# Kernel optimization log

Measured on AMD Instinct MI355X. Metric: run time of the kernel, lower is better.

Reference implementation:

```python
import jax, jax.numpy as jnp
import numpy as np

E = 512       # embed_dim
H = 8         # num_heads
DH = E // H   # head dim
F = 2048      # dim_feedforward
KS = 33       # NATTEN kernel_size (dilation=1)
NCLS = 1
B = 2
L = 4096      # local tokens (total seq = L + NCLS)
EPS = 1e-5


def layernorm(x, g, b):
    mu = jnp.mean(x, axis=-1, keepdims=True)
    var = jnp.mean(jnp.square(x - mu), axis=-1, keepdims=True)
    return (x - mu) * jax.lax.rsqrt(var + EPS) * g + b


def natten_1d(x, qkv_w, qkv_b, proj_w, proj_b):
    # Neighborhood attention 1D, dilation=1, non-causal, no rel-pos bias.
    b, l, e = x.shape
    qkv = x @ qkv_w.T + qkv_b                       # [b, l, 3E]
    q, k, v = jnp.split(qkv, 3, axis=-1)
    q = q.reshape(b, l, H, DH) * (DH ** -0.5)
    k = k.reshape(b, l, H, DH)
    v = v.reshape(b, l, H, DH)
    # NATTEN window: centered, shifted at edges to keep exactly KS in-bounds neighbors
    starts = jnp.clip(jnp.arange(l) - KS // 2, 0, l - KS)   # [l]
    idx = starts[:, None] + jnp.arange(KS)                  # [l, KS]
    kn = k[:, idx]                                          # [b, l, KS, H, DH]
    vn = v[:, idx]                                          # [b, l, KS, H, DH]
    attn = jnp.einsum('blhd,blkhd->bhlk', q, kn)
    attn = jax.nn.softmax(attn, axis=-1)
    out = jnp.einsum('bhlk,blkhd->blhd', attn, vn).reshape(b, l, e)
    return out @ proj_w.T + proj_b


def global_mha(q_in, kv_in, in_w, in_b, out_w, out_b):
    # torch nn.MultiheadAttention, batch_first, no masks
    bq, lq, e = q_in.shape
    lk = kv_in.shape[1]
    wq, wk, wv = jnp.split(in_w, 3, axis=0)
    bqp, bkp, bvp = jnp.split(in_b, 3, axis=0)
    q = (q_in @ wq.T + bqp).reshape(bq, lq, H, DH) * (DH ** -0.5)
    k = (kv_in @ wk.T + bkp).reshape(bq, lk, H, DH)
    v = (kv_in @ wv.T + bvp).reshape(bq, lk, H, DH)
    attn = jax.nn.softmax(jnp.einsum('bqhd,bkhd->bhqk', q, k), axis=-1)
    out = jnp.einsum('bhqk,bkhd->bqhd', attn, v).reshape(bq, lq, e)
    return out @ out_w.T + out_b


def setup_inputs() -> dict:
    key = jax.random.key(0)
    ks = jax.random.split(key, 16)
    s = 0.02
    return {
        'x': jax.random.normal(ks[0], (B, L + NCLS, E), jnp.float32),
        'ln1_g': jnp.ones((E,), jnp.float32),
        'ln1_b': jnp.zeros((E,), jnp.float32),
        'qkv_w': jax.random.normal(ks[1], (3 * E, E), jnp.float32) * s,
        'qkv_b': jnp.zeros((3 * E,), jnp.float32),
        'na_proj_w': jax.random.normal(ks[2], (E, E), jnp.float32) * s,
        'na_proj_b': jnp.zeros((E,), jnp.float32),
        'in_proj_w': jax.random.normal(ks[3], (3 * E, E), jnp.float32) * s,
        'in_proj_b': jnp.zeros((3 * E,), jnp.float32),
        'out_w': jax.random.normal(ks[4], (E, E), jnp.float32) * s,
        'out_b': jnp.zeros((E,), jnp.float32),
        'ln2_g': jnp.ones((E,), jnp.float32),
        'ln2_b': jnp.zeros((E,), jnp.float32),
        'fc1_w': jax.random.normal(ks[5], (F, E), jnp.float32) * s,
        'fc1_b': jnp.zeros((F,), jnp.float32),
        'fc2_w': jax.random.normal(ks[6], (E, F), jnp.float32) * s,
        'fc2_b': jnp.zeros((E,), jnp.float32),
    }


def reference(x, ln1_g, ln1_b, qkv_w, qkv_b, na_proj_w, na_proj_b,
              in_proj_w, in_proj_b, out_w, out_b, ln2_g, ln2_b,
              fc1_w, fc1_b, fc2_w, fc2_b):
    res = x
    xn = layernorm(x, ln1_g, ln1_b)
    x_local = natten_1d(xn[:, :-NCLS, :], qkv_w, qkv_b, na_proj_w, na_proj_b)
    tmp_key = jnp.concatenate([x_local, xn[:, -NCLS:, :]], axis=1)
    x_cls = global_mha(xn[:, -NCLS:, :], tmp_key, in_proj_w, in_proj_b, out_w, out_b)
    x = res + jnp.concatenate([x_local, x_cls], axis=1)
    res = x
    xn = layernorm(x, ln2_g, ln2_b)
    h = jax.nn.silu(xn @ fc1_w.T + fc1_b)
    return res + (h @ fc2_w.T + fc2_b)
```

## Files before the change

### kernel.cpp

```cpp
#include <hip/hip_runtime.h>
#include <hip/hip_bf16.h>
#include <cstdint>
#include <cstddef>

#define E    512
#define H    8
#define DHD  64
#define FDIM 2048
#define KS   33
#define BB   2
#define LL   4096
#define LP1  4097
#define NTOK 8194
#define NLOC 8192

typedef unsigned short ushort_t;
typedef __bf16 bf16x8_t __attribute__((ext_vector_type(8)));
typedef float  f32x4_t  __attribute__((ext_vector_type(4)));

__device__ __forceinline__ float b2f(unsigned short h) {
  union { unsigned int u; float f; } un; un.u = ((unsigned int)h) << 16; return un.f;
}
__device__ __forceinline__ unsigned short f2b(float f) {
  union { float f; unsigned int u; } un; un.f = f;
  unsigned int u = un.u;
  return (unsigned short)((u + 0x7FFFu + ((u >> 16) & 1u)) >> 16);
}

__device__ __forceinline__ void gload16(const ushort_t* g, ushort_t* l) {
  __builtin_amdgcn_global_load_lds(
      (const __attribute__((address_space(1))) void*)g,
      (__attribute__((address_space(3))) void*)l,
      16, 0, 0);
}

template<int N> __device__ __forceinline__ void waitcnt_vm() {
  if constexpr (N == 8)      asm volatile("s_waitcnt vmcnt(8)" ::: "memory");
  else if constexpr (N == 6) asm volatile("s_waitcnt vmcnt(6)" ::: "memory");
  else                       asm volatile("s_waitcnt vmcnt(0)" ::: "memory");
}

__device__ __forceinline__ int xcd_remap(int hw, int n) {
  int xcd = hw & 7, j = hw >> 3;
  int q = n >> 3, r = n & 7;
  return (xcd < r ? xcd * (q + 1) : r * (q + 1) + (xcd - r) * q) + j;
}

template<int BMT, int BNT, int NTH, int WC, int ACT, int OUTF, int ADDRES,
         int INRM, int OUTRM, int PARTIAL>
__global__ __launch_bounds__(NTH) void gemm_bt(
    const ushort_t* __restrict__ A, const ushort_t* __restrict__ W,
    const float* __restrict__ bias, float* __restrict__ outF,
    ushort_t* __restrict__ outB, const ushort_t* __restrict__ res,
    int M, int N, int K, int klen, int ny, int nz, size_t pstr)
{
  constexpr int WR  = NTH / 64 / WC;
  constexpr int MF  = BMT / (WR * 16);
  constexpr int NF  = BNT / (WC * 16);
  constexpr int AR  = (BMT * 64) / (8 * NTH);
  constexpr int BR  = (BNT * 64) / (8 * NTH);
  constexpr int RPR = NTH / 8;
  constexpr int NLD = AR + BR;
  __shared__ ushort_t Alds[2][BMT * 64];
  __shared__ ushort_t Blds[2][BNT * 64];
  const int t    = threadIdx.x;
  const int lane = t & 63;
  const int w    = t >> 6;
  const int wr   = w / WC, wc = w % WC;

  const int Lid = xcd_remap(blockIdx.x, gridDim.x);
  const int bx  = Lid / (ny * nz);
  const int rem = Lid % (ny * nz);
  const int z   = rem / ny;
  const int by  = rem % ny;
  const int bmBase = bx * BMT;
  const int bnBase = by * BNT;
  const int kbeg = z * klen;

  f32x4_t zero = {0.f, 0.f, 0.f, 0.f};
  f32x4_t acc[MF][NF];
  #pragma unroll
  for (int m = 0; m < MF; ++m)
    #pragma unroll
    for (int n = 0; n < NF; ++n) acc[m][n] = zero;

  const int srow = t >> 3;
  const int jsw8 = ((t & 7) ^ (srow & 7)) * 8;
  int arow[AR];
  #pragma unroll
  for (int r = 0; r < AR; ++r) {
    int rr = bmBase + r * RPR + srow;
    if (INRM) rr += rr >> 12;
    else if (rr >= M) rr = M - 1;
    arow[r] = rr;
  }
  int brow[BR];
  #pragma unroll
  for (int r = 0; r < BR; ++r) brow[r] = bnBase + r * RPR + srow;

  const int frow = lane & 15;
  const int g    = lane >> 4;

  auto STAGE = [&](int s, int k0) {
    #pragma unroll
    for (int r = 0; r < AR; ++r)
      gload16(A + (size_t)arow[r] * K + k0 + jsw8, &Alds[s][(size_t)(r * NTH + t) * 8]);
    #pragma unroll
    for (int r = 0; r < BR; ++r)
      gload16(W + (size_t)brow[r] * K + k0 + jsw8, &Blds[s][(size_t)(r * NTH + t) * 8]);
  };

  const int nt = klen >> 6;
  STAGE(0, kbeg);
  if (nt > 1) STAGE(1, kbeg + 64);

  for (int it = 0; it < nt; ++it) {
    const int cur = it & 1;
    if (it < nt - 1) waitcnt_vm<NLD>();
    else             waitcnt_vm<0>();
    __builtin_amdgcn_s_barrier();
    #pragma unroll
    for (int kk2 = 0; kk2 < 2; ++kk2) {
      bf16x8_t af[MF], bfv[NF];
      const int kosw = ((kk2 * 4 + g) ^ (frow & 7)) << 4;
      #pragma unroll
      for (int m = 0; m < MF; ++m) {
        int row = wr * (MF * 16) + m * 16 + frow;
        af[m] = *reinterpret_cast<const bf16x8_t*>((char*)Alds[cur] + row * 128 + kosw);
      }
      #pragma unroll
      for (int n = 0; n < NF; ++n) {
        int row = wc * (NF * 16) + n * 16 + frow;
        bfv[n] = *reinterpret_cast<const bf16x8_t*>((char*)Blds[cur] + row * 128 + kosw);
      }
      #pragma unroll
      for (int m = 0; m < MF; ++m)
        #pragma unroll
        for (int n = 0; n < NF; ++n)
          acc[m][n] = __builtin_amdgcn_mfma_f32_16x16x32_bf16(af[m], bfv[n], acc[m][n], 0, 0, 0);
    }
    __builtin_amdgcn_s_barrier();
    if (it + 2 < nt) STAGE(cur, kbeg + (it + 2) * 64);
  }

  const int rbase = g * 4;
  const int cbase = frow;
  #pragma unroll
  for (int m = 0; m < MF; ++m) {
    #pragma unroll
    for (int r = 0; r < 4; ++r) {
      int gr = bmBase + wr * (MF * 16) + m * 16 + rbase + r;
      if (gr < M) {
        int orow = OUTRM ? gr + (gr >> 12) : gr;
        #pragma unroll
        for (int n = 0; n < NF; ++n) {
          int gc = bnBase + wc * (NF * 16) + n * 16 + cbase;
          float v = acc[m][n][r];
          if (PARTIAL) {
            outB[(size_t)z * pstr + (size_t)orow * N + gc] = f2b(v);
          } else {
            v += bias[gc];
            if (ACT == 1) v = v / (1.f + __expf(-v));
            if (ADDRES) v += b2f(res[(size_t)gr * N + gc]);
            if (OUTF) outF[(size_t)orow * N + gc] = v;
            else      outB[(size_t)orow * N + gc] = f2b(v);
          }
        }
      }
    }
  }
}

template<int NP>
__global__ __launch_bounds__(256) void fc2_reduce(
    float* __restrict__ out, const ushort_t* __restrict__ parts, size_t pstr,
    const float* __restrict__ bias, const ushort_t* __restrict__ xab)
{
  size_t i4 = (size_t)blockIdx.x * 256 + threadIdx.x;
  ushort4 xv = reinterpret_cast<const ushort4*>(xab)[i4];
  float4 bcol = reinterpret_cast<const float4*>(bias)[i4 & 127];
  float4 o;
  o.x = b2f(xv.x) + bcol.x; o.y = b2f(xv.y) + bcol.y;
  o.z = b2f(xv.z) + bcol.z; o.w = b2f(xv.w) + bcol.w;
  #pragma unroll
  for (int zp = 0; zp < NP; ++zp) {
    ushort4 pv = *reinterpret_cast<const ushort4*>(parts + (size_t)zp * pstr + i4 * 4);
    o.x += b2f(pv.x); o.y += b2f(pv.y); o.z += b2f(pv.z); o.w += b2f(pv.w);
  }
  reinterpret_cast<float4*>(out)[i4] = o;
}

__global__ __launch_bounds__(256) void ln_fused1(
    const float* __restrict__ x, const float* __restrict__ g,
    const float* __restrict__ be, ushort_t* __restrict__ xn,
    ushort_t* __restrict__ tmpk)
{
  __shared__ float sh[4];
  const int row = blockIdx.x;
  const int t = threadIdx.x;
  const float* xr = x + (size_t)row * E;
  float v0 = xr[t], v1 = xr[t + 256];
  float sum = v0 + v1;
  #pragma unroll
  for (int o = 32; o; o >>= 1) sum += __shfl_xor(sum, o);
  if ((t & 63) == 0) sh[t >> 6] = sum;
  __syncthreads();
  float mean = (sh[0] + sh[1] + sh[2] + sh[3]) * (1.f / E);
  __syncthreads();
  float d0 = v0 - mean, d1 = v1 - mean;
  float vs = d0 * d0 + d1 * d1;
  #pragma unroll
  for (int o = 32; o; o >>= 1) vs += __shfl_xor(vs, o);
  if ((t & 63) == 0) sh[t >> 6] = vs;
  __syncthreads();
  float var = (sh[0] + sh[1] + sh[2] + sh[3]) * (1.f / E);
  float rstd = rsqrtf(var + 1e-5f);
  unsigned short o0 = f2b(d0 * rstd * g[t] + be[t]);
  unsigned short o1 = f2b(d1 * rstd * g[t + 256] + be[t + 256]);
  xn[(size_t)row * E + t] = o0;
  xn[(size_t)row * E + t + 256] = o1;
  if ((row % LP1) == LL) {
    tmpk[(size_t)row * E + t] = o0;
    tmpk[(size_t)row * E + t + 256] = o1;
  }
}

__global__ __launch_bounds__(256) void resid_ln2(
    const float* __restrict__ x, const ushort_t* __restrict__ tmpk,
    const float* __restrict__ xcls, const float* __restrict__ g,
    const float* __restrict__ be, ushort_t* __restrict__ xab,
    ushort_t* __restrict__ xn2)
{
  __shared__ float sh[4];
  const int row = blockIdx.x;
  const int b = row / LP1, l = row % LP1;
  const int t = threadIdx.x;
  float a0, a1;
  if (l < LL) { a0 = b2f(tmpk[(size_t)row * E + t]); a1 = b2f(tmpk[(size_t)row * E + t + 256]); }
  else        { a0 = xcls[b * E + t];                a1 = xcls[b * E + t + 256]; }
  float v0 = x[(size_t)row * E + t] + a0;
  float v1 = x[(size_t)row * E + t + 256] + a1;
  xab[(size_t)row * E + t] = f2b(v0);
  xab[(size_t)row * E + t + 256] = f2b(v1);
  float sum = v0 + v1;
  #pragma unroll
  for (int o = 32; o; o >>= 1) sum += __shfl_xor(sum, o);
  if ((t & 63) == 0) sh[t >> 6] = sum;
  __syncthreads();
  float mean = (sh[0] + sh[1] + sh[2] + sh[3]) * (1.f / E);
  __syncthreads();
  float d0 = v0 - mean, d1 = v1 - mean;
  float vs = d0 * d0 + d1 * d1;
  #pragma unroll
  for (int o = 32; o; o >>= 1) vs += __shfl_xor(vs, o);
  if ((t & 63) == 0) sh[t >> 6] = vs;
  __syncthreads();
  float var = (sh[0] + sh[1] + sh[2] + sh[3]) * (1.f / E);
  float rstd = rsqrtf(var + 1e-5f);
  xn2[(size_t)row * E + t]       = f2b(d0 * rstd * g[t] + be[t]);
  xn2[(size_t)row * E + t + 256] = f2b(d1 * rstd * g[t + 256] + be[t + 256]);
}

__global__ __launch_bounds__(256) void natten_mfma(
    const ushort_t* __restrict__ qkv, ushort_t* __restrict__ out)
{
  __shared__ ushort_t KP[4][64 * 64];
  __shared__ ushort_t VT[4][64 * 72];
  const int w    = threadIdx.x >> 6;
  const int lane = threadIdx.x & 63;
  const int task = blockIdx.x * 4 + w;
  const int h  = task & 7;
  const int qb = (task >> 3) & 127;
  const int b  = task >> 10;
  const int l0 = qb * 32;
  const int kb = l0 - 16;
  const ushort_t* base = qkv + (size_t)b * LL * (3 * E);
  ushort_t* Klds = KP[w];
  ushort_t* Vt   = VT[w];

  {
    const int rsub = lane >> 3;
    const int d0   = (lane & 7) * 8;
    #pragma unroll
    for (int i = 0; i < 8; ++i) {
      int row = i * 8 + rsub;
      int gl = kb + row; gl = gl < 0 ? 0 : (gl > LL - 1 ? LL - 1 : gl);
      bf16x8_t kv = *reinterpret_cast<const bf16x8_t*>(
          base + (size_t)gl * (3 * E) + E + h * 64 + d0);
      int ba = (row * 128 + d0 * 2) ^ ((row & 7) << 4);
      *reinterpret_cast<bf16x8_t*>((char*)Klds + ba) = kv;
    }
  }
  {
    const int a  = lane & 7;
    const int c8 = lane >> 3;
    unsigned int* Vt32 = (unsigned int*)Vt;
    #pragma unroll
    for (int i = 0; i < 4; ++i) {
      int rp = i * 8 + c8;
      int g0 = kb + rp * 2;     g0 = g0 < 0 ? 0 : (g0 > LL - 1 ? LL - 1 : g0);
      int g1 = kb + rp * 2 + 1; g1 = g1 < 0 ? 0 : (g1 > LL - 1 ? LL - 1 : g1);
      const ushort_t* v0 = base + (size_t)g0 * (3 * E) + 2 * E + h * 64 + a * 8;
      const ushort_t* v1 = base + (size_t)g1 * (3 * E) + 2 * E + h * 64 + a * 8;
      ushort4 x0 = *(const ushort4*)v0,       x1 = *(const ushort4*)v1;
      ushort4 y0 = *(const ushort4*)(v0 + 4), y1 = *(const ushort4*)(v1 + 4);
      int d = a * 8;
      Vt32[(d + 0) * 36 + rp] = (unsigned)x0.x | ((unsigned)x1.x << 16);
      Vt32[(d + 1) * 36 + rp] = (unsigned)x0.y | ((unsigned)x1.y << 16);
      Vt32[(d + 2) * 36 + rp] = (unsigned)x0.z | ((unsigned)x1.z << 16);
      Vt32[(d + 3) * 36 + rp] = (unsigned)x0.w | ((unsigned)x1.w << 16);
      Vt32[(d + 4) * 36 + rp] = (unsigned)y0.x | ((unsigned)y1.x << 16);
      Vt32[(d + 5) * 36 + rp] = (unsigned)y0.y | ((unsigned)y1.y << 16);
      Vt32[(d + 6) * 36 + rp] = (unsigned)y0.z | ((unsigned)y1.z << 16);
      Vt32[(d + 7) * 36 + rp] = (unsigned)y0.w | ((unsigned)y1.w << 16);
    }
  }

  const int p = lane & 15, g = lane >> 4;
  bf16x8_t qf[2][2];
  #pragma unroll
  for (int mt = 0; mt < 2; ++mt)
    #pragma unroll
    for (int ks = 0; ks < 2; ++ks)
      qf[mt][ks] = *reinterpret_cast<const bf16x8_t*>(
          base + (size_t)(l0 + mt * 16 + p) * (3 * E) + h * 64 + ks * 32 + g * 8);

  f32x4_t zero = {0.f, 0.f, 0.f, 0.f};
  f32x4_t accS[2][4];
  #pragma unroll
  for (int mt = 0; mt < 2; ++mt)
    #pragma unroll
    for (int nt = 0; nt < 4; ++nt) accS[mt][nt] = zero;
  #pragma unroll
  for (int ks = 0; ks < 2; ++ks) {
    bf16x8_t kf[4];
    #pragma unroll
    for (int nt = 0; nt < 4; ++nt) {
      int row = nt * 16 + p;
      int ba = (row * 128 + (ks * 32 + g * 8) * 2) ^ ((row & 7) << 4);
      kf[nt] = *reinterpret_cast<const bf16x8_t*>((char*)Klds + ba);
    }
    #pragma unroll
    for (int mt = 0; mt < 2; ++mt)
      #pragma unroll
      for (int nt = 0; nt < 4; ++nt)
        accS[mt][nt] = __builtin_amdgcn_mfma_f32_16x16x32_bf16(qf[mt][ks], kf[nt], accS[mt][nt], 0, 0, 0);
  }

  ushort_t* Plds = Klds;
  #pragma unroll
  for (int mt = 0; mt < 2; ++mt) {
    #pragma unroll
    for (int r = 0; r < 4; ++r) {
      int lq = l0 + mt * 16 + g * 4 + r;
      int st = lq - 16; st = st < 0 ? 0 : (st > LL - KS ? LL - KS : st);
      int clo = st - kb, chi = clo + 32;
      float sv[4];
      float mx = -1e30f;
      #pragma unroll
      for (int nt = 0; nt < 4; ++nt) {
        int c = nt * 16 + p;
        float s = accS[mt][nt][r] * 0.125f;
        s = (c >= clo && c <= chi) ? s : -1e30f;
        sv[nt] = s;
        mx = fmaxf(mx, s);
      }
      mx = fmaxf(mx, __shfl_xor(mx, 1));
      mx = fmaxf(mx, __shfl_xor(mx, 2));
      mx = fmaxf(mx, __shfl_xor(mx, 4));
      mx = fmaxf(mx, __shfl_xor(mx, 8));
      float sum = 0.f;
      #pragma unroll
      for (int nt = 0; nt < 4; ++nt) { float e = __expf(sv[nt] - mx); sv[nt] = e; sum += e; }
      sum += __shfl_xor(sum, 1);
      sum += __shfl_xor(sum, 2);
      sum += __shfl_xor(sum, 4);
      sum += __shfl_xor(sum, 8);
      float inv = 1.f / sum;
      int q = mt * 16 + g * 4 + r;
      #pragma unroll
      for (int nt = 0; nt < 4; ++nt)
        Plds[q * 72 + nt * 16 + p] = f2b(sv[nt] * inv);
    }
  }

  f32x4_t accO[2][4];
  #pragma unroll
  for (int mt = 0; mt < 2; ++mt)
    #pragma unroll
    for (int nt = 0; nt < 4; ++nt) accO[mt][nt] = zero;
  #pragma unroll
  for (int ks = 0; ks < 2; ++ks) {
    bf16x8_t pf[2], vf[4];
    #pragma unroll
    for (int mt = 0; mt < 2; ++mt)
      pf[mt] = *reinterpret_cast<const bf16x8_t*>(
          (char*)Plds + (mt * 16 + p) * 144 + (ks * 32 + g * 8) * 2);
    #pragma unroll
    for (int nt = 0; nt < 4; ++nt)
      vf[nt] = *reinterpret_cast<const bf16x8_t*>(
          (char*)Vt + (nt * 16 + p) * 144 + (ks * 32 + g * 8) * 2);
    #pragma unroll
    for (int mt = 0; mt < 2; ++mt)
      #pragma unroll
      for (int nt = 0; nt < 4; ++nt)
        accO[mt][nt] = __builtin_amdgcn_mfma_f32_16x16x32_bf16(pf[mt], vf[nt], accO[mt][nt], 0, 0, 0);
  }

  #pragma unroll
  for (int mt = 0; mt < 2; ++mt) {
    #pragma unroll
    for (int r = 0; r < 4; ++r) {
      int lq = l0 + mt * 16 + g * 4 + r;
      ushort_t* orow = out + ((size_t)(b * LL) + lq) * E + h * 64;
      #pragma unroll
      for (int nt = 0; nt < 4; ++nt)
        orow[nt * 16 + p] = f2b(accO[mt][nt][r]);
    }
  }
}

__global__ __launch_bounds__(256) void qcls_kernel(
    const ushort_t* __restrict__ xn, const float* __restrict__ inw,
    const float* __restrict__ inb, float* __restrict__ qcls)
{
  int i = blockIdx.x * 256 + threadIdx.x;
  int b = i >> 9, d = i & 511;
  const ushort_t* xr = xn + ((size_t)b * LP1 + LL) * E;
  const float* wr = inw + (size_t)d * E;
  float s = 0.f;
  for (int e = 0; e < E; e += 4) {
    ushort4 xv = *reinterpret_cast<const ushort4*>(xr + e);
    s += b2f(xv.x) * wr[e] + b2f(xv.y) * wr[e + 1] + b2f(xv.z) * wr[e + 2] + b2f(xv.w) * wr[e + 3];
  }
  qcls[i] = (s + inb[d]) * 0.125f;
}

__global__ __launch_bounds__(256) void gscore_kernel(
    const float* __restrict__ qcls, const ushort_t* __restrict__ kv,
    float* __restrict__ sc)
{
  const int wav = blockIdx.x * 4 + (threadIdx.x >> 6);
  if (wav >= BB * LP1) return;
  const int lane = threadIdx.x & 63;
  const int b = wav / LP1, j = wav % LP1;
  const ushort_t* kr = kv + (size_t)wav * 1024 + lane * 8;
  const float* q = qcls + b * E + lane * 8;
  ushort4 ka = *reinterpret_cast<const ushort4*>(kr);
  ushort4 kb4 = *reinterpret_cast<const ushort4*>(kr + 4);
  float s = b2f(ka.x) * q[0] + b2f(ka.y) * q[1] + b2f(ka.z) * q[2] + b2f(ka.w) * q[3]
          + b2f(kb4.x) * q[4] + b2f(kb4.y) * q[5] + b2f(kb4.z) * q[6] + b2f(kb4.w) * q[7];
  s += __shfl_xor(s, 1); s += __shfl_xor(s, 2); s += __shfl_xor(s, 4);
  if ((lane & 7) == 0) sc[((size_t)(b * 8) + (lane >> 3)) * LP1 + j] = s;
}

__global__ __launch_bounds__(256) void gsoftmax_kernel(float* __restrict__ sc)
{
  float* row = sc + (size_t)blockIdx.x * LP1;
  __shared__ float sh[4];
  const int t = threadIdx.x;
  float m = -1e30f;
  for (int i = t; i < LP1; i += 256) m = fmaxf(m, row[i]);
  #pragma unroll
  for (int o = 32; o; o >>= 1) m = fmaxf(m, __shfl_xor(m, o));
  if ((t & 63) == 0) sh[t >> 6] = m;
  __syncthreads();
  m = fmaxf(fmaxf(sh[0], sh[1]), fmaxf(sh[2], sh[3]));
  __syncthreads();
  float s = 0.f;
  for (int i = t; i < LP1; i += 256) { float e = __expf(row[i] - m); row[i] = e; s += e; }
  #pragma unroll
  for (int o = 32; o; o >>= 1) s += __shfl_xor(s, o);
  if ((t & 63) == 0) sh[t >> 6] = s;
  __syncthreads();
  float inv = 1.f / (sh[0] + sh[1] + sh[2] + sh[3]);
  for (int i = t; i < LP1; i += 256) row[i] *= inv;
}

__global__ __launch_bounds__(256) void gpv_kernel(
    const float* __restrict__ sc, const ushort_t* __restrict__ kv,
    float* __restrict__ parts)
{
  __shared__ float red[4][64];
  const int bh = blockIdx.y;
  const int b = bh >> 3, h = bh & 7;
  const int c = blockIdx.x;
  const int lane = threadIdx.x & 63, s4 = threadIdx.x >> 6;
  const int j0 = c * 512;
  const int jend = (j0 + 512 < LP1) ? j0 + 512 : LP1;
  const float* prow = sc + (size_t)bh * LP1;
  const ushort_t* vbase = kv + (size_t)b * LP1 * 1024 + 512 + h * 64 + lane;
  float acc = 0.f;
  for (int j = j0 + s4; j < jend; j += 4)
    acc += prow[j] * b2f(vbase[(size_t)j * 1024]);
  red[s4][lane] = acc;
  __syncthreads();
  if (s4 == 0)
    parts[((size_t)c * 16 + bh) * 64 + lane] = red[0][lane] + red[1][lane] + red[2][lane] + red[3][lane];
}

__global__ void gpv_reduce(const float* __restrict__ parts, float* __restrict__ oc)
{
  int i = blockIdx.x * 256 + threadIdx.x;
  if (i < BB * E) {
    float s = 0.f;
    #pragma unroll
    for (int c = 0; c < 9; ++c) s += parts[c * 1024 + i];
    oc[i] = s;
  }
}

__global__ __launch_bounds__(256) void xcls_kernel(
    const float* __restrict__ oc, const float* __restrict__ ow,
    const float* __restrict__ ob, float* __restrict__ xc)
{
  int i = blockIdx.x * 256 + threadIdx.x;
  if (i >= BB * E) return;
  int b = i >> 9, n = i & 511;
  const float* o = oc + b * E;
  const float* wr = ow + (size_t)n * E;
  float s = ob[n];
  for (int m = 0; m < E; ++m) s += o[m] * wr[m];
  xc[i] = s;
}

__global__ void cvt_all(
    const float* __restrict__ s0, ushort_t* __restrict__ d0, int n0,
    const float* __restrict__ s1, ushort_t* __restrict__ d1, int n1,
    const float* __restrict__ s2, ushort_t* __restrict__ d2, int n2,
    const float* __restrict__ s3, ushort_t* __restrict__ d3, int n3,
    const float* __restrict__ s4, ushort_t* __restrict__ d4, int n4)
{
  int i = (blockIdx.x * 256 + threadIdx.x) * 4;
  const float* s; ushort_t* d;
  if (i < n0)                { s = s0; d = d0; }
  else if ((i -= n0) < n1)   { s = s1; d = d1; }
  else if ((i -= n1) < n2)   { s = s2; d = d2; }
  else if ((i -= n2) < n3)   { s = s3; d = d3; }
  else if ((i -= n3) < n4)   { s = s4; d = d4; }
  else return;
  float4 v = *reinterpret_cast<const float4*>(s + i);
  ushort4 o;
  o.x = f2b(v.x); o.y = f2b(v.y); o.z = f2b(v.z); o.w = f2b(v.w);
  *reinterpret_cast<ushort4*>(d + i) = o;
}

extern "C" void kernel_launch(void* const* d_in, const int* in_sizes, int n_in,
                              void* d_out, int out_size, void* d_ws, size_t ws_size,
                              hipStream_t stream)
{
  const float* x      = (const float*)d_in[0];
  const float* ln1_g  = (const float*)d_in[1];
  const float* ln1_b  = (const float*)d_in[2];
  const float* qkv_w  = (const float*)d_in[3];
  const float* qkv_b  = (const float*)d_in[4];
  const float* na_w   = (const float*)d_in[5];
  const float* na_b   = (const float*)d_in[6];
  const float* in_w   = (const float*)d_in[7];
  const float* in_b   = (const float*)d_in[8];
  const float* out_w  = (const float*)d_in[9];
  const float* out_b  = (const float*)d_in[10];
  const float* ln2_g  = (const float*)d_in[11];
  const float* ln2_b  = (const float*)d_in[12];
  const float* fc1_w  = (const float*)d_in[13];
  const float* fc1_b  = (const float*)d_in[14];
  const float* fc2_w  = (const float*)d_in[15];
  const float* fc2_b  = (const float*)d_in[16];
  float* out = (float*)d_out;

  char* pws = (char*)d_ws;
  size_t off = 0;
  auto alloc = [&](size_t bytes) {
    void* r = pws + off; off = (off + bytes + 255) & ~(size_t)255; return r;
  };
  ushort_t* w_qkv = (ushort_t*)alloc((size_t)3 * E * E * 2);
  ushort_t* w_na  = (ushort_t*)alloc((size_t)E * E * 2);
  ushort_t* w_in  = (ushort_t*)alloc((size_t)3 * E * E * 2);
  ushort_t* w_fc1 = (ushort_t*)alloc((size_t)FDIM * E * 2);
  ushort_t* w_fc2 = (ushort_t*)alloc((size_t)E * FDIM * 2);
  ushort_t* xn1   = (ushort_t*)alloc((size_t)NTOK * E * 2);
  char*     bigR  = (char*)alloc((size_t)NTOK * FDIM * 2);
  ushort_t* qkvb  = (ushort_t*)bigR;
  ushort_t* natt  = (ushort_t*)(bigR + (size_t)NLOC * 3 * E * 2);
  ushort_t* kvg   = (ushort_t*)bigR;
  ushort_t* hbuf  = (ushort_t*)bigR;
  ushort_t* tmpk  = (ushort_t*)alloc((size_t)NTOK * E * 2);
  float*    sc    = (float*)alloc((size_t)BB * H * LP1 * 4);
  float*    qcls  = (float*)alloc(1024 * 4);
  float*    parts = (float*)alloc(9 * 16 * 64 * 4);
  float*    oc    = (float*)alloc(1024 * 4);
  float*    xcls  = (float*)alloc(1024 * 4);
  ushort_t* xab   = (ushort_t*)alloc((size_t)NTOK * E * 2);
  ushort_t* xn2   = xn1;
  const size_t PS = (size_t)NTOK * E;
  size_t off_save = off;
  ushort_t* sk = (ushort_t*)alloc(4 * PS * 2);
  int nsplit = 4;
  if (off > ws_size) {
    off = off_save;
    sk = (ushort_t*)alloc(2 * PS * 2);
    nsplit = 2;
    if (off > ws_size) { off = off_save; nsplit = 1; }
  }

  cvt_all<<<3840, 256, 0, stream>>>(
      qkv_w, w_qkv, 3 * E * E,
      na_w,  w_na,  E * E,
      in_w,  w_in,  3 * E * E,
      fc1_w, w_fc1, FDIM * E,
      fc2_w, w_fc2, E * FDIM);

  ln_fused1<<<NTOK, 256, 0, stream>>>(x, ln1_g, ln1_b, xn1, tmpk);
  qcls_kernel<<<4, 256, 0, stream>>>(xn1, in_w, in_b, qcls);
  gemm_bt<256,256,512,4, 0,0,0,1,0,0><<<192, 512, 0, stream>>>(
      xn1, w_qkv, qkv_b, nullptr, qkvb, nullptr, NLOC, 3 * E, E, E, 6, 1, 0);
  natten_mfma<<<512, 256, 0, stream>>>(qkvb, natt);
  gemm_bt<128,64,256,2, 0,0,0,0,1,0><<<512, 256, 0, stream>>>(
      natt, w_na, na_b, nullptr, tmpk, nullptr, NLOC, E, E, E, 8, 1, 0);
  gemm_bt<128,128,256,2, 0,0,0,0,0,0><<<520, 256, 0, stream>>>(
      tmpk, w_in + (size_t)E * E, in_b + E, nullptr, kvg, nullptr, NTOK, 1024, E, E, 8, 1, 0);
  gscore_kernel<<<(BB * LP1 + 3) / 4, 256, 0, stream>>>(qcls, kvg, sc);
  gsoftmax_kernel<<<BB * H, 256, 0, stream>>>(sc);
  gpv_kernel<<<dim3(9, BB * H), 256, 0, stream>>>(sc, kvg, parts);
  gpv_reduce<<<4, 256, 0, stream>>>(parts, oc);
  xcls_kernel<<<4, 256, 0, stream>>>(oc, out_w, out_b, xcls);
  resid_ln2<<<NTOK, 256, 0, stream>>>(x, tmpk, xcls, ln2_g, ln2_b, xab, xn2);
  gemm_bt<256,128,512,4, 1,0,0,0,0,0><<<528, 512, 0, stream>>>(
      xn2, w_fc1, fc1_b, nullptr, hbuf, nullptr, NTOK, FDIM, E, E, 16, 1, 0);
  if (nsplit == 4) {
    gemm_bt<256,128,512,4, 0,0,0,0,0,1><<<528, 512, 0, stream>>>(
        hbuf, w_fc2, fc2_b, nullptr, sk, nullptr, NTOK, E, FDIM, FDIM / 4, 4, 4, PS);
    fc2_reduce<4><<<(NTOK * E / 4) / 256, 256, 0, stream>>>(out, sk, PS, fc2_b, xab);
  } else if (nsplit == 2) {
    gemm_bt<256,128,512,4, 0,0,0,0,0,1><<<33 * 4 * 2, 512, 0, stream>>>(
        hbuf, w_fc2, fc2_b, nullptr, sk, nullptr, NTOK, E, FDIM, FDIM / 2, 4, 2, PS);
    fc2_reduce<2><<<(NTOK * E / 4) / 256, 256, 0, stream>>>(out, sk, PS, fc2_b, xab);
  } else {
    gemm_bt<256,128,512,4, 0,1,1,0,0,0><<<33 * 4, 512, 0, stream>>>(
        hbuf, w_fc2, fc2_b, out, nullptr, xab, NTOK, E, FDIM, FDIM, 4, 1, 0);
  }
}
```

Before: 292.8 us.

## Replace GEMMs with 256x256 eight-wave kernel using quarter-tile interleaved staging

Introduces a new 256x256-tile, 512-thread GEMM that splits each K-step into four quadrant phases. Half-tile global-to-LDS loads are interleaved with the MFMA work, using fine-grained vmcnt waits, barriers and raised wave priority. It is applied to the QKV, KV-projection, fc1 and fc2 GEMMs with adjusted grids. The NA projection instead uses a simpler single-buffered 128x64 kernel. This aims to raise reuse and overlap memory with compute, at the cost of fewer blocks on the smaller GEMMs (e.g. 132 blocks for the KV GEMM) and heavy register and LDS use.

```diff
diff --git a/kernel.cpp b/kernel.cpp
--- a/kernel.cpp
+++ b/kernel.cpp
@@ -35,9 +35,7 @@
 }
 
 template<int N> __device__ __forceinline__ void waitcnt_vm() {
-  if constexpr (N == 8)      asm volatile("s_waitcnt vmcnt(8)" ::: "memory");
-  else if constexpr (N == 6) asm volatile("s_waitcnt vmcnt(6)" ::: "memory");
-  else                       asm volatile("s_waitcnt vmcnt(0)" ::: "memory");
+  asm volatile("s_waitcnt vmcnt(%0)" :: "n"(N) : "memory");
 }
 
 __device__ __forceinline__ int xcd_remap(int hw, int n) {
@@ -46,36 +44,180 @@
   return (xcd < r ? xcd * (q + 1) : r * (q + 1) + (xcd - r) * q) + j;
 }
 
-template<int BMT, int BNT, int NTH, int WC, int ACT, int OUTF, int ADDRES,
-         int INRM, int OUTRM, int PARTIAL>
-__global__ __launch_bounds__(NTH) void gemm_bt(
+template<int ACT, int OUTF, int ADDRES, int INRM, int PARTIAL>
+__global__ __launch_bounds__(512) void gemm8p(
     const ushort_t* __restrict__ A, const ushort_t* __restrict__ W,
     const float* __restrict__ bias, float* __restrict__ outF,
     ushort_t* __restrict__ outB, const ushort_t* __restrict__ res,
     int M, int N, int K, int klen, int ny, int nz, size_t pstr)
 {
-  constexpr int WR  = NTH / 64 / WC;
-  constexpr int MF  = BMT / (WR * 16);
-  constexpr int NF  = BNT / (WC * 16);
-  constexpr int AR  = (BMT * 64) / (8 * NTH);
-  constexpr int BR  = (BNT * 64) / (8 * NTH);
-  constexpr int RPR = NTH / 8;
-  constexpr int NLD = AR + BR;
-  __shared__ ushort_t Alds[2][BMT * 64];
-  __shared__ ushort_t Blds[2][BNT * 64];
+  __shared__ ushort_t Al[2][256 * 64];
+  __shared__ ushort_t Bl[2][256 * 64];
   const int t    = threadIdx.x;
   const int lane = t & 63;
   const int w    = t >> 6;
-  const int wr   = w / WC, wc = w % WC;
+  const int wr   = (w >> 2) & 1, wc = w & 3;
 
   const int Lid = xcd_remap(blockIdx.x, gridDim.x);
   const int bx  = Lid / (ny * nz);
   const int rem = Lid % (ny * nz);
   const int z   = rem / ny;
   const int by  = rem % ny;
-  const int bmBase = bx * BMT;
+  const int bmBase = bx * 256;
+  const int bnBase = by * 256;
+  const int kbeg = z * klen;
+
+  f32x4_t zero = {0.f, 0.f, 0.f, 0.f};
+  f32x4_t acc[8][4];
+  #pragma unroll
+  for (int m = 0; m < 8; ++m)
+    #pragma unroll
+    for (int n = 0; n < 4; ++n) acc[m][n] = zero;
+
+  const int srow = t >> 3;
+  const int jsw8 = ((t & 7) ^ (srow & 7)) * 8;
+  const int frow = lane & 15;
+  const int g    = lane >> 4;
+
+  auto STAGE_A = [&](int s, int h, int k0) {
+    #pragma unroll
+    for (int r = 0; r < 2; ++r) {
+      int row = h * 128 + r * 64 + srow;
+      int rr = bmBase + row;
+      if (INRM) rr += rr >> 12;
+      else if (rr >= M) rr = M - 1;
+      gload16(A + (size_t)rr * K + k0 + jsw8, &Al[s][(size_t)row * 64 + (t & 7) * 8]);
+    }
+  };
+  auto STAGE_B = [&](int s, int h, int k0) {
+    #pragma unroll
+    for (int r = 0; r < 2; ++r) {
+      int row = h * 128 + r * 64 + srow;
+      gload16(W + (size_t)(bnBase + row) * K + k0 + jsw8,
+              &Bl[s][(size_t)row * 64 + (t & 7) * 8]);
+    }
+  };
+
+  const int NTt = klen >> 6;
+  STAGE_A(0, 0, kbeg);
+  STAGE_B(0, 0, kbeg);
+  STAGE_A(0, 1, kbeg);
+  STAGE_B(0, 1, kbeg);
+  if (NTt > 1) {
+    STAGE_A(1, 0, kbeg + 64);
+    STAGE_B(1, 0, kbeg + 64);
+    waitcnt_vm<8>();
+  } else {
+    waitcnt_vm<4>();
+  }
+  __builtin_amdgcn_s_barrier();
+
+  for (int kt = 0; kt < NTt; ++kt) {
+    const int cb = kt & 1;
+    const int k1 = kbeg + (kt + 1) * 64;
+    const int k2 = kbeg + (kt + 2) * 64;
+    const int wsel = (kt < NTt - 2) ? 0 : ((kt == NTt - 2) ? 1 : 2);
+    #pragma unroll
+    for (int q = 0; q < 4; ++q) {
+      const int qm = q >> 1, qn = q & 1;
+      bf16x8_t af[4][2], bf[2][2];
+      #pragma unroll
+      for (int m = 0; m < 4; ++m) {
+        const int row = qm * 128 + wr * 64 + m * 16 + frow;
+        const char* rp = (const char*)Al[cb] + row * 128;
+        af[m][0] = *(const bf16x8_t*)(rp + (((g    ) ^ (row & 7)) << 4));
+        af[m][1] = *(const bf16x8_t*)(rp + (((4 + g) ^ (row & 7)) << 4));
+      }
+      #pragma unroll
+      for (int n = 0; n < 2; ++n) {
+        const int row = qn * 128 + wc * 32 + n * 16 + frow;
+        const char* rp = (const char*)Bl[cb] + row * 128;
+        bf[n][0] = *(const bf16x8_t*)(rp + (((g    ) ^ (row & 7)) << 4));
+        bf[n][1] = *(const bf16x8_t*)(rp + (((4 + g) ^ (row & 7)) << 4));
+      }
+      if (q == 0) { if (kt + 1 < NTt) STAGE_A(cb ^ 1, 1, k1); }
+      if (q == 1) { if (kt + 1 < NTt) STAGE_B(cb ^ 1, 1, k1); }
+      if (q == 2) { if (kt + 2 < NTt) STAGE_A(cb, 0, k2); }
+      if (q == 3) { if (kt + 2 < NTt) STAGE_B(cb, 0, k2); }
+      if (wsel == 0) {
+        if (q == 0) waitcnt_vm<6>();
+        else if (q == 1) waitcnt_vm<10>();
+        else if (q == 2) waitcnt_vm<10>();
+        else waitcnt_vm<8>();
+      } else if (wsel == 1) {
+        if (q == 0) waitcnt_vm<6>();
+        else if (q == 1) waitcnt_vm<10>();
+        else if (q == 2) waitcnt_vm<8>();
+        else waitcnt_vm<4>();
+      } else {
+        waitcnt_vm<0>();
+      }
+      __builtin_amdgcn_s_barrier();
+      asm volatile("s_waitcnt lgkmcnt(0)" ::: "memory");
+      __builtin_amdgcn_sched_barrier(0);
+      __builtin_amdgcn_s_setprio(1);
+      #pragma unroll
+      for (int m = 0; m < 4; ++m)
+        #pragma unroll
+        for (int n = 0; n < 2; ++n) {
+          acc[qm * 4 + m][qn * 2 + n] =
+              __builtin_amdgcn_mfma_f32_16x16x32_bf16(af[m][0], bf[n][0], acc[qm * 4 + m][qn * 2 + n], 0, 0, 0);
+          acc[qm * 4 + m][qn * 2 + n] =
+              __builtin_amdgcn_mfma_f32_16x16x32_bf16(af[m][1], bf[n][1], acc[qm * 4 + m][qn * 2 + n], 0, 0, 0);
+        }
+      __builtin_amdgcn_s_setprio(0);
+      __builtin_amdgcn_s_barrier();
+    }
+  }
+
+  const int rbase = g * 4;
+  #pragma unroll
+  for (int m = 0; m < 8; ++m) {
+    const int qm = m >> 2, ml = m & 3;
+    #pragma unroll
+    for (int r = 0; r < 4; ++r) {
+      int gr = bmBase + qm * 128 + wr * 64 + ml * 16 + rbase + r;
+      if (gr < M) {
+        #pragma unroll
+        for (int n = 0; n < 4; ++n) {
+          const int qn = n >> 1, nl = n & 1;
+          int gc = bnBase + qn * 128 + wc * 32 + nl * 16 + frow;
+          float v = acc[m][n][r];
+          if (PARTIAL) {
+            outB[(size_t)z * pstr + (size_t)gr * N + gc] = f2b(v);
+          } else {
+            v += bias[gc];
+            if (ACT == 1) v = v / (1.f + __expf(-v));
+            if (ADDRES) v += b2f(res[(size_t)gr * N + gc]);
+            if (OUTF) outF[(size_t)gr * N + gc] = v;
+            else      outB[(size_t)gr * N + gc] = f2b(v);
+          }
+        }
+      }
+    }
+  }
+}
+
+template<int BNT, int WC, int OUTRM>
+__global__ __launch_bounds__(256) void gemm_old(
+    const ushort_t* __restrict__ A, const ushort_t* __restrict__ W,
+    const float* __restrict__ bias, ushort_t* __restrict__ outB,
+    int M, int N, int K, int ny)
+{
+  constexpr int MF = 4;
+  constexpr int NF = BNT / (WC * 16);
+  constexpr int BR = (BNT * 64) / (8 * 256);
+  __shared__ ushort_t Alds[128 * 64];
+  __shared__ ushort_t Blds[BNT * 64];
+  const int t    = threadIdx.x;
+  const int lane = t & 63;
+  const int w    = t >> 6;
+  const int wr   = w / WC, wc = w % WC;
+  const int Lid = xcd_remap(blockIdx.x, gridDim.x);
+  const int bx  = Lid / ny;
+  const int by  = Lid % ny;
+  const int bmBase = bx * 128;
   const int bnBase = by * BNT;
-  const int kbeg = z * klen;
 
   f32x4_t zero = {0.f, 0.f, 0.f, 0.f};
   f32x4_t acc[MF][NF];
@@ -86,52 +228,41 @@
 
   const int srow = t >> 3;
   const int jsw8 = ((t & 7) ^ (srow & 7)) * 8;
-  int arow[AR];
-  #pragma unroll
-  for (int r = 0; r < AR; ++r) {
-    int rr = bmBase + r * RPR + srow;
-    if (INRM) rr += rr >> 12;
-    else if (rr >= M) rr = M - 1;
+  int arow[4];
+  #pragma unroll
+  for (int r = 0; r < 4; ++r) {
+    int rr = bmBase + r * 32 + srow;
+    if (rr >= M) rr = M - 1;
     arow[r] = rr;
   }
   int brow[BR];
   #pragma unroll
-  for (int r = 0; r < BR; ++r) brow[r] = bnBase + r * RPR + srow;
+  for (int r = 0; r < BR; ++r) brow[r] = bnBase + r * 32 + srow;
 
   const int frow = lane & 15;
   const int g    = lane >> 4;
 
-  auto STAGE = [&](int s, int k0) {
-    #pragma unroll
-    for (int r = 0; r < AR; ++r)
-      gload16(A + (size_t)arow[r] * K + k0 + jsw8, &Alds[s][(size_t)(r * NTH + t) * 8]);
+  for (int k0 = 0; k0 < K; k0 += 64) {
+    #pragma unroll
+    for (int r = 0; r < 4; ++r)
+      gload16(A + (size_t)arow[r] * K + k0 + jsw8, &Alds[(size_t)(r * 256 + t) * 8]);
     #pragma unroll
     for (int r = 0; r < BR; ++r)
-      gload16(W + (size_t)brow[r] * K + k0 + jsw8, &Blds[s][(size_t)(r * NTH + t) * 8]);
-  };
-
-  const int nt = klen >> 6;
-  STAGE(0, kbeg);
-  if (nt > 1) STAGE(1, kbeg + 64);
-
-  for (int it = 0; it < nt; ++it) {
-    const int cur = it & 1;
-    if (it < nt - 1) waitcnt_vm<NLD>();
-    else             waitcnt_vm<0>();
-    __builtin_amdgcn_s_barrier();
+      gload16(W + (size_t)brow[r] * K + k0 + jsw8, &Blds[(size_t)(r * 256 + t) * 8]);
+    __syncthreads();
     #pragma unroll
     for (int kk2 = 0; kk2 < 2; ++kk2) {
       bf16x8_t af[MF], bfv[NF];
       const int kosw = ((kk2 * 4 + g) ^ (frow & 7)) << 4;
       #pragma unroll
       for (int m = 0; m < MF; ++m) {
-        int row = wr * (MF * 16) + m * 16 + frow;
-        af[m] = *reinterpret_cast<const bf16x8_t*>((char*)Alds[cur] + row * 128 + kosw);
+        int row = wr * 64 + m * 16 + frow;
+        af[m] = *reinterpret_cast<const bf16x8_t*>((char*)Alds + row * 128 + kosw);
       }
       #pragma unroll
       for (int n = 0; n < NF; ++n) {
         int row = wc * (NF * 16) + n * 16 + frow;
-        bfv[n] = *reinterpret_cast<const bf16x8_t*>((char*)Blds[cur] + row * 128 + kosw);
+        bfv[n] = *reinterpret_cast<const bf16x8_t*>((char*)Blds + row * 128 + kosw);
       }
       #pragma unroll
       for (int m = 0; m < MF; ++m)
@@ -139,32 +270,21 @@
         for (int n = 0; n < NF; ++n)
           acc[m][n] = __builtin_amdgcn_mfma_f32_16x16x32_bf16(af[m], bfv[n], acc[m][n], 0, 0, 0);
     }
-    __builtin_amdgcn_s_barrier();
-    if (it + 2 < nt) STAGE(cur, kbeg + (it + 2) * 64);
+    __syncthreads();
   }
 
   const int rbase = g * 4;
-  const int cbase = frow;
   #pragma unroll
   for (int m = 0; m < MF; ++m) {
     #pragma unroll
     for (int r = 0; r < 4; ++r) {
-      int gr = bmBase + wr * (MF * 16) + m * 16 + rbase + r;
+      int gr = bmBase + wr * 64 + m * 16 + rbase + r;
       if (gr < M) {
         int orow = OUTRM ? gr + (gr >> 12) : gr;
         #pragma unroll
         for (int n = 0; n < NF; ++n) {
-          int gc = bnBase + wc * (NF * 16) + n * 16 + cbase;
-          float v = acc[m][n][r];
-          if (PARTIAL) {
-            outB[(size_t)z * pstr + (size_t)orow * N + gc] = f2b(v);
-          } else {
-            v += bias[gc];
-            if (ACT == 1) v = v / (1.f + __expf(-v));
-            if (ADDRES) v += b2f(res[(size_t)gr * N + gc]);
-            if (OUTF) outF[(size_t)orow * N + gc] = v;
-            else      outB[(size_t)orow * N + gc] = f2b(v);
-          }
+          int gc = bnBase + wc * (NF * 16) + n * 16 + frow;
+          outB[(size_t)orow * N + gc] = f2b(acc[m][n][r] + bias[gc]);
         }
       }
     }
@@ -612,31 +732,31 @@
 
   ln_fused1<<<NTOK, 256, 0, stream>>>(x, ln1_g, ln1_b, xn1, tmpk);
   qcls_kernel<<<4, 256, 0, stream>>>(xn1, in_w, in_b, qcls);
-  gemm_bt<256,256,512,4, 0,0,0,1,0,0><<<192, 512, 0, stream>>>(
+  gemm8p<0,0,0,1,0><<<192, 512, 0, stream>>>(
       xn1, w_qkv, qkv_b, nullptr, qkvb, nullptr, NLOC, 3 * E, E, E, 6, 1, 0);
   natten_mfma<<<512, 256, 0, stream>>>(qkvb, natt);
-  gemm_bt<128,64,256,2, 0,0,0,0,1,0><<<512, 256, 0, stream>>>(
-      natt, w_na, na_b, nullptr, tmpk, nullptr, NLOC, E, E, E, 8, 1, 0);
-  gemm_bt<128,128,256,2, 0,0,0,0,0,0><<<520, 256, 0, stream>>>(
-      tmpk, w_in + (size_t)E * E, in_b + E, nullptr, kvg, nullptr, NTOK, 1024, E, E, 8, 1, 0);
+  gemm_old<64,2,1><<<512, 256, 0, stream>>>(
+      natt, w_na, na_b, tmpk, NLOC, E, E, 8);
+  gemm8p<0,0,0,0,0><<<132, 512, 0, stream>>>(
+      tmpk, w_in + (size_t)E * E, in_b + E, nullptr, kvg, nullptr, NTOK, 1024, E, E, 4, 1, 0);
   gscore_kernel<<<(BB * LP1 + 3) / 4, 256, 0, stream>>>(qcls, kvg, sc);
   gsoftmax_kernel<<<BB * H, 256, 0, stream>>>(sc);
   gpv_kernel<<<dim3(9, BB * H), 256, 0, stream>>>(sc, kvg, parts);
   gpv_reduce<<<4, 256, 0, stream>>>(parts, oc);
   xcls_kernel<<<4, 256, 0, stream>>>(oc, out_w, out_b, xcls);
   resid_ln2<<<NTOK, 256, 0, stream>>>(x, tmpk, xcls, ln2_g, ln2_b, xab, xn2);
-  gemm_bt<256,128,512,4, 1,0,0,0,0,0><<<528, 512, 0, stream>>>(
-      xn2, w_fc1, fc1_b, nullptr, hbuf, nullptr, NTOK, FDIM, E, E, 16, 1, 0);
+  gemm8p<1,0,0,0,0><<<264, 512, 0, stream>>>(
+      xn2, w_fc1, fc1_b, nullptr, hbuf, nullptr, NTOK, FDIM, E, E, 8, 1, 0);
   if (nsplit == 4) {
-    gemm_bt<256,128,512,4, 0,0,0,0,0,1><<<528, 512, 0, stream>>>(
-        hbuf, w_fc2, fc2_b, nullptr, sk, nullptr, NTOK, E, FDIM, FDIM / 4, 4, 4, PS);
+    gemm8p<0,0,0,0,1><<<33 * 2 * 4, 512, 0, stream>>>(
+        hbuf, w_fc2, fc2_b, nullptr, sk, nullptr, NTOK, E, FDIM, FDIM / 4, 2, 4, PS);
     fc2_reduce<4><<<(NTOK * E / 4) / 256, 256, 0, stream>>>(out, sk, PS, fc2_b, xab);
   } else if (nsplit == 2) {
-    gemm_bt<256,128,512,4, 0,0,0,0,0,1><<<33 * 4 * 2, 512, 0, stream>>>(
-        hbuf, w_fc2, fc2_b, nullptr, sk, nullptr, NTOK, E, FDIM, FDIM / 2, 4, 2, PS);
+    gemm8p<0,0,0,0,1><<<33 * 2 * 2, 512, 0, stream>>>(
+        hbuf, w_fc2, fc2_b, nullptr, sk, nullptr, NTOK, E, FDIM, FDIM / 2, 2, 2, PS);
     fc2_reduce<2><<<(NTOK * E / 4) / 256, 256, 0, stream>>>(out, sk, PS, fc2_b, xab);
   } else {
-    gemm_bt<256,128,512,4, 0,1,1,0,0,0><<<33 * 4, 512, 0, stream>>>(
-        hbuf, w_fc2, fc2_b, out, nullptr, xab, NTOK, E, FDIM, FDIM, 4, 1, 0);
-  }
-}
+    gemm8p<0,1,1,0,0><<<33 * 2, 512, 0, stream>>>(
+        hbuf, w_fc2, fc2_b, out, nullptr, xab, NTOK, E, FDIM, FDIM, 2, 1, 0);
+  }
+}
```

Result: slower. 311.5 us (+6.4%).
